# Kernel tuning notes

Measured on AMD Instinct MI355X. Metric: run time of the kernel, lower is better.

Reference implementation:

```python
import jax, jax.numpy as jnp
import numpy as np

N_NODES = 10000
N_EDGES = 640000
D_NODE = 128
D_EDGE = 64
D_IN = D_NODE + D_EDGE  # 192
D_OUT = 128


def setup_inputs() -> dict:
    key = jax.random.key(0)
    k1, k2, k3, k4 = jax.random.split(key, 4)
    x = jax.random.normal(k1, (N_NODES, D_NODE), dtype=jnp.float32)
    edge_index = jax.random.randint(k2, (2, N_EDGES), 0, N_NODES, dtype=jnp.int64)
    edge_features = jax.random.normal(k3, (N_EDGES, D_EDGE), dtype=jnp.float32)
    W = jax.random.normal(k4, (D_IN, D_OUT), dtype=jnp.float32) * (1.0 / np.sqrt(D_IN))
    b = jnp.zeros((D_OUT,), dtype=jnp.float32)
    return {"x": x, "edge_index": edge_index, "edge_features": edge_features, "W": W, "b": b}


def reference(x, edge_index, edge_features, W, b):
    n_nodes = x.shape[0]
    src = edge_index[0]  # [E]
    dst = edge_index[1]  # [E]
    # gather source node feats, concat edge feats, linear
    h = jnp.concatenate([x[src], edge_features], axis=1)  # [E, D_IN]
    h = h @ W + b  # [E, D_OUT]
    # scatter-mean to destination nodes
    sums = jax.ops.segment_sum(h, dst, num_segments=n_nodes)  # [N, D_OUT]
    cnt = jax.ops.segment_sum(jnp.ones((h.shape[0],), dtype=h.dtype), dst, num_segments=n_nodes)
    return sums / jnp.maximum(cnt, 1.0)[:, None]
```

## Files before the change

kernel.cpp:

```cpp
#include <hip/hip_runtime.h>

#define D_NODE 128
#define D_EDGE 64
#define D_IN 192
#define D_OUT 128

static __device__ __forceinline__ unsigned f2bf(float f) {
    unsigned u = __float_as_uint(f);
    return (u + 0x7fffu + ((u >> 16) & 1u)) >> 16;
}


__global__ void k_rank(const int* __restrict__ dst, int* __restrict__ cnt,
                       int* __restrict__ rank, const float2* __restrict__ x2,
                       unsigned* __restrict__ xb, int nx2, int E) {
    int e = blockIdx.x * 256 + threadIdx.x;
    if (e < E) rank[e] = atomicAdd(&cnt[dst[e]], 1);
    if (e < nx2) {
        float2 v = x2[e];
        xb[e] = f2bf(v.x) | (f2bf(v.y) << 16);
    }
}

__global__ __launch_bounds__(1024) void k_scan(const int* __restrict__ cnt,
                                               int* __restrict__ offsets, int N) {
    __shared__ int wsum[16];
    int tid = threadIdx.x;
    int lane = tid & 63, wid = tid >> 6;
    const int CH = (N + 1023) / 1024;
    int i0 = tid * CH;
    int local[16];
    int lsum = 0;
    for (int c = 0; c < CH; ++c) {
        int i = i0 + c;
        int v = (i < N) ? cnt[i] : 0;
        local[c] = v;
        lsum += v;
    }
    int incl = lsum;
    for (int off = 1; off < 64; off <<= 1) {
        int t = __shfl_up(incl, off, 64);
        if (lane >= off) incl += t;
    }
    if (lane == 63) wsum[wid] = incl;
    __syncthreads();
    if (wid == 0) {
        int s = (lane < 16) ? wsum[lane] : 0;
        for (int off = 1; off < 16; off <<= 1) {
            int t = __shfl_up(s, off, 64);
            if (lane >= off) s += t;
        }
        if (lane < 16) wsum[lane] = s;
    }
    __syncthreads();
    int waveoff = (wid > 0) ? wsum[wid - 1] : 0;
    int run = waveoff + incl - lsum;
    for (int c = 0; c < CH; ++c) {
        int i = i0 + c;
        if (i < N) { offsets[i] = run; run += local[c]; }
    }
    if (tid == 0) offsets[N] = wsum[15];
}

__global__ void k_place(const int* __restrict__ ei, const int* __restrict__ offsets,
                        const int* __restrict__ rank, int2* __restrict__ csr, int E) {
    int i = blockIdx.x * 256 + threadIdx.x;
    int e = i * 4;
    if (e + 4 <= E) {
        int4 s4 = *(const int4*)(ei + e);
        int4 d4 = *(const int4*)(ei + E + e);
        int4 r4 = *(const int4*)(rank + e);
        csr[offsets[d4.x] + r4.x] = make_int2(s4.x, e + 0);
        csr[offsets[d4.y] + r4.y] = make_int2(s4.y, e + 1);
        csr[offsets[d4.z] + r4.z] = make_int2(s4.z, e + 2);
        csr[offsets[d4.w] + r4.w] = make_int2(s4.w, e + 3);
    } else {
        for (; e < E; ++e)
            csr[offsets[ei[E + e]] + rank[e]] = make_int2(ei[e], e);
    }
}

__global__ __launch_bounds__(256) void k_gather(
        const unsigned* __restrict__ xb, const float* __restrict__ ef,
        const int* __restrict__ offsets, const int2* __restrict__ csr,
        float* __restrict__ agg, int N) {
    int wid = threadIdx.x >> 6;
    int lane = threadIdx.x & 63;
    int node = blockIdx.x * 4 + wid;
    if (node >= N) return;
    int start = offsets[node];
    int end = offsets[node + 1];
    float ax[4] = {0.f, 0.f, 0.f, 0.f};
    float ay[4] = {0.f, 0.f, 0.f, 0.f};
    float az[4] = {0.f, 0.f, 0.f, 0.f};
    for (int base = start; base < end; base += 64) {
        int m = end - base;
        if (m > 64) m = 64;
        int2 ent = make_int2(0, 0);
        if (lane < m) {
            long long raw = __builtin_nontemporal_load((const long long*)(csr + base + lane));
            ent.x = (int)(raw & 0xffffffffLL);
            ent.y = (int)(raw >> 32);
        }
        int j = 0;
        for (; j + 8 <= m; j += 8) {
            unsigned xv[8];
            float    ev[8];
#pragma unroll
            for (int u = 0; u < 8; ++u) {
                int s  = __shfl(ent.x, j + u, 64);
                int id = __shfl(ent.y, j + u, 64);
                xv[u] = xb[(unsigned)s * 64u + lane];
                ev[u] = __builtin_nontemporal_load(ef + (unsigned)id * 64u + lane);
            }
#pragma unroll
            for (int u = 0; u < 8; ++u) {
                ax[u & 3] += __uint_as_float(xv[u] << 16);
                ay[u & 3] += __uint_as_float(xv[u] & 0xffff0000u);
                az[u & 3] += ev[u];
            }
        }
        for (; j < m; ++j) {
            int s  = __shfl(ent.x, j, 64);
            int id = __shfl(ent.y, j, 64);
            unsigned xv = xb[(unsigned)s * 64u + lane];
            float    ev = __builtin_nontemporal_load(ef + (unsigned)id * 64u + lane);
            ax[0] += __uint_as_float(xv << 16);
            ay[0] += __uint_as_float(xv & 0xffff0000u);
            az[0] += ev;
        }
    }
    float a0 = (ax[0] + ax[1]) + (ax[2] + ax[3]);
    float a1 = (ay[0] + ay[1]) + (ay[2] + ay[3]);
    float a2 = (az[0] + az[1]) + (az[2] + az[3]);
    float2* aggrow = (float2*)(agg + (size_t)node * D_IN);
    aggrow[lane] = make_float2(a0, a1);
    agg[(size_t)node * D_IN + 128 + lane] = a2;
}

__global__ __launch_bounds__(256) void k_gemm(
        const float* __restrict__ agg, const float* __restrict__ W,
        const float* __restrict__ b, const int* __restrict__ offsets,
        float* __restrict__ out, int N) {
    __shared__ float sAgg[16][D_IN];
    __shared__ int scnt[16];
    int tid = threadIdx.x;
    int n0 = blockIdx.x * 16;
    for (int i = tid; i < 16 * D_IN; i += 256) {
        int m = i / D_IN;
        int k = i - m * D_IN;
        int n = n0 + m;
        sAgg[m][k] = (n < N) ? agg[(size_t)n * D_IN + k] : 0.0f;
    }
    if (tid < 16) {
        int n = n0 + tid;
        scnt[tid] = (n < N) ? (offsets[n + 1] - offsets[n]) : 0;
    }
    __syncthreads();
    int o = tid & 127;
    int g = tid >> 7;
    float acc[8];
#pragma unroll
    for (int m = 0; m < 8; ++m) acc[m] = 0.0f;
    for (int k = 0; k < D_IN; k += 4) {
        float w0 = W[(k + 0) * D_OUT + o];
        float w1 = W[(k + 1) * D_OUT + o];
        float w2 = W[(k + 2) * D_OUT + o];
        float w3 = W[(k + 3) * D_OUT + o];
#pragma unroll
        for (int m = 0; m < 8; ++m) {
            const float4 av = *(const float4*)(&sAgg[g * 8 + m][k]);
            acc[m] += av.x * w0 + av.y * w1 + av.z * w2 + av.w * w3;
        }
    }
    float bo = b[o];
#pragma unroll
    for (int m = 0; m < 8; ++m) {
        int n = n0 + g * 8 + m;
        if (n < N) {
            int c = scnt[g * 8 + m];
            float v = (c > 0) ? (acc[m] / (float)c + bo) : 0.0f;
            __builtin_nontemporal_store(v, &out[(size_t)n * D_OUT + o]);
        }
    }
}

extern "C" void kernel_launch(void* const* d_in, const int* in_sizes, int n_in,
                              void* d_out, int out_size, void* d_ws, size_t ws_size,
                              hipStream_t stream) {
    const float* x  = (const float*)d_in[0];
    const int*   ei = (const int*)d_in[1];
    const float* ef = (const float*)d_in[2];
    const float* W  = (const float*)d_in[3];
    const float* b  = (const float*)d_in[4];
    float* out = (float*)d_out;

    const int N = in_sizes[0] / D_NODE;
    const int E = in_sizes[2] / D_EDGE;
    const int nx2 = in_sizes[0] / 2;

    auto align64 = [](size_t v) { return (v + 63) & ~(size_t)63; };
    char* ws = (char*)d_ws;
    size_t o_cnt = 0;
    size_t o_off = align64(o_cnt + (size_t)N * 4);
    size_t o_rnk = align64(o_off + (size_t)(N + 1) * 4);
    size_t o_csr = align64(o_rnk + (size_t)E * 4);
    size_t o_xb  = align64(o_csr + (size_t)E * 8);
    size_t o_agg = align64(o_xb + (size_t)nx2 * 4);
    int*  cnt     = (int*)(ws + o_cnt);
    int*  offsets = (int*)(ws + o_off);
    int*  rank    = (int*)(ws + o_rnk);
    int2* csr     = (int2*)(ws + o_csr);
    unsigned* xb  = (unsigned*)(ws + o_xb);
    float* agg    = (float*)(ws + o_agg);

    int gridR = ((E > nx2 ? E : nx2) + 255) / 256;
    hipMemsetAsync(cnt, 0, (size_t)N * 4, stream);
    k_rank<<<gridR, 256, 0, stream>>>(ei + E, cnt, rank, (const float2*)x, xb, nx2, E);
    k_scan<<<1, 1024, 0, stream>>>(cnt, offsets, N);
    k_place<<<(E / 4 + 255) / 256, 256, 0, stream>>>(ei, offsets, rank, csr, E);
    k_gather<<<(N + 3) / 4, 256, 0, stream>>>(xb, ef, offsets, csr, agg, N);
    k_gemm<<<(N + 15) / 16, 256, 0, stream>>>(agg, W, b, offsets, out, N);
}
```

Before: 326.4 us.

## Fuse all stages into one persistent kernel with grid barriers

Replaces five kernel launches with a single persistent kernel of 512 blocks that uses atomic-counter grid barriers between the count, scan, CSR-place, and gather+GEMM phases. The gather now writes aggregated rows directly into shared memory and immediately runs the GEMM, eliminating the global agg buffer round trip. This removes launch overheads and the intermediate store/load, but it relies on all 512 blocks being co-resident, serializes the scan onto one 256-thread block, and reduces gather parallelism (4 waves per 16-node chunk).

Measured after the change: 870.4 us. 2.67x slower.

```diff
diff --git a/kernel.cpp b/kernel.cpp
--- a/kernel.cpp
+++ b/kernel.cpp
@@ -4,183 +4,184 @@
 #define D_EDGE 64
 #define D_IN 192
 #define D_OUT 128
+#define NBLK 512
 
 static __device__ __forceinline__ unsigned f2bf(float f) {
     unsigned u = __float_as_uint(f);
     return (u + 0x7fffu + ((u >> 16) & 1u)) >> 16;
 }
 
-
-__global__ void k_rank(const int* __restrict__ dst, int* __restrict__ cnt,
-                       int* __restrict__ rank, const float2* __restrict__ x2,
-                       unsigned* __restrict__ xb, int nx2, int E) {
-    int e = blockIdx.x * 256 + threadIdx.x;
-    if (e < E) rank[e] = atomicAdd(&cnt[dst[e]], 1);
-    if (e < nx2) {
-        float2 v = x2[e];
-        xb[e] = f2bf(v.x) | (f2bf(v.y) << 16);
-    }
-}
-
-__global__ __launch_bounds__(1024) void k_scan(const int* __restrict__ cnt,
-                                               int* __restrict__ offsets, int N) {
-    __shared__ int wsum[16];
-    int tid = threadIdx.x;
-    int lane = tid & 63, wid = tid >> 6;
-    const int CH = (N + 1023) / 1024;
-    int i0 = tid * CH;
-    int local[16];
-    int lsum = 0;
-    for (int c = 0; c < CH; ++c) {
-        int i = i0 + c;
-        int v = (i < N) ? cnt[i] : 0;
-        local[c] = v;
-        lsum += v;
-    }
-    int incl = lsum;
-    for (int off = 1; off < 64; off <<= 1) {
-        int t = __shfl_up(incl, off, 64);
-        if (lane >= off) incl += t;
-    }
-    if (lane == 63) wsum[wid] = incl;
+static __device__ __forceinline__ void grid_barrier(int* ctr, int nblocks) {
     __syncthreads();
-    if (wid == 0) {
-        int s = (lane < 16) ? wsum[lane] : 0;
-        for (int off = 1; off < 16; off <<= 1) {
-            int t = __shfl_up(s, off, 64);
-            if (lane >= off) s += t;
-        }
-        if (lane < 16) wsum[lane] = s;
+    if (threadIdx.x == 0) {
+        __threadfence();
+        __hip_atomic_fetch_add(ctr, 1, __ATOMIC_ACQ_REL, __HIP_MEMORY_SCOPE_AGENT);
+        while (__hip_atomic_load(ctr, __ATOMIC_ACQUIRE, __HIP_MEMORY_SCOPE_AGENT) < nblocks) {
+            __builtin_amdgcn_s_sleep(2);
+        }
+        __threadfence();
     }
     __syncthreads();
-    int waveoff = (wid > 0) ? wsum[wid - 1] : 0;
-    int run = waveoff + incl - lsum;
-    for (int c = 0; c < CH; ++c) {
-        int i = i0 + c;
-        if (i < N) { offsets[i] = run; run += local[c]; }
-    }
-    if (tid == 0) offsets[N] = wsum[15];
-}
-
-__global__ void k_place(const int* __restrict__ ei, const int* __restrict__ offsets,
-                        const int* __restrict__ rank, int2* __restrict__ csr, int E) {
-    int i = blockIdx.x * 256 + threadIdx.x;
-    int e = i * 4;
-    if (e + 4 <= E) {
-        int4 s4 = *(const int4*)(ei + e);
-        int4 d4 = *(const int4*)(ei + E + e);
-        int4 r4 = *(const int4*)(rank + e);
-        csr[offsets[d4.x] + r4.x] = make_int2(s4.x, e + 0);
-        csr[offsets[d4.y] + r4.y] = make_int2(s4.y, e + 1);
-        csr[offsets[d4.z] + r4.z] = make_int2(s4.z, e + 2);
-        csr[offsets[d4.w] + r4.w] = make_int2(s4.w, e + 3);
-    } else {
-        for (; e < E; ++e)
-            csr[offsets[ei[E + e]] + rank[e]] = make_int2(ei[e], e);
-    }
-}
-
-__global__ __launch_bounds__(256) void k_gather(
-        const unsigned* __restrict__ xb, const float* __restrict__ ef,
-        const int* __restrict__ offsets, const int2* __restrict__ csr,
-        float* __restrict__ agg, int N) {
-    int wid = threadIdx.x >> 6;
-    int lane = threadIdx.x & 63;
-    int node = blockIdx.x * 4 + wid;
-    if (node >= N) return;
-    int start = offsets[node];
-    int end = offsets[node + 1];
-    float ax[4] = {0.f, 0.f, 0.f, 0.f};
-    float ay[4] = {0.f, 0.f, 0.f, 0.f};
-    float az[4] = {0.f, 0.f, 0.f, 0.f};
-    for (int base = start; base < end; base += 64) {
-        int m = end - base;
-        if (m > 64) m = 64;
-        int2 ent = make_int2(0, 0);
-        if (lane < m) {
-            long long raw = __builtin_nontemporal_load((const long long*)(csr + base + lane));
-            ent.x = (int)(raw & 0xffffffffLL);
-            ent.y = (int)(raw >> 32);
-        }
-        int j = 0;
-        for (; j + 8 <= m; j += 8) {
-            unsigned xv[8];
-            float    ev[8];
-#pragma unroll
-            for (int u = 0; u < 8; ++u) {
-                int s  = __shfl(ent.x, j + u, 64);
-                int id = __shfl(ent.y, j + u, 64);
-                xv[u] = xb[(unsigned)s * 64u + lane];
-                ev[u] = __builtin_nontemporal_load(ef + (unsigned)id * 64u + lane);
-            }
-#pragma unroll
-            for (int u = 0; u < 8; ++u) {
-                ax[u & 3] += __uint_as_float(xv[u] << 16);
-                ay[u & 3] += __uint_as_float(xv[u] & 0xffff0000u);
-                az[u & 3] += ev[u];
-            }
-        }
-        for (; j < m; ++j) {
-            int s  = __shfl(ent.x, j, 64);
-            int id = __shfl(ent.y, j, 64);
-            unsigned xv = xb[(unsigned)s * 64u + lane];
-            float    ev = __builtin_nontemporal_load(ef + (unsigned)id * 64u + lane);
-            ax[0] += __uint_as_float(xv << 16);
-            ay[0] += __uint_as_float(xv & 0xffff0000u);
-            az[0] += ev;
-        }
-    }
-    float a0 = (ax[0] + ax[1]) + (ax[2] + ax[3]);
-    float a1 = (ay[0] + ay[1]) + (ay[2] + ay[3]);
-    float a2 = (az[0] + az[1]) + (az[2] + az[3]);
-    float2* aggrow = (float2*)(agg + (size_t)node * D_IN);
-    aggrow[lane] = make_float2(a0, a1);
-    agg[(size_t)node * D_IN + 128 + lane] = a2;
-}
-
-__global__ __launch_bounds__(256) void k_gemm(
-        const float* __restrict__ agg, const float* __restrict__ W,
-        const float* __restrict__ b, const int* __restrict__ offsets,
-        float* __restrict__ out, int N) {
+}
+
+__global__ __launch_bounds__(256, 4) void k_fused(
+        const int* __restrict__ ei,
+        const float2* __restrict__ x2, int nx2,
+        const float* __restrict__ ef,
+        const float* __restrict__ W, const float* __restrict__ b,
+        int* __restrict__ cnt, int* __restrict__ ctr,
+        int* __restrict__ offsets, int* __restrict__ rank,
+        int2* __restrict__ csr, unsigned* __restrict__ xb,
+        float* __restrict__ out, int N, int E) {
     __shared__ float sAgg[16][D_IN];
     __shared__ int scnt[16];
-    int tid = threadIdx.x;
-    int n0 = blockIdx.x * 16;
-    for (int i = tid; i < 16 * D_IN; i += 256) {
-        int m = i / D_IN;
-        int k = i - m * D_IN;
-        int n = n0 + m;
-        sAgg[m][k] = (n < N) ? agg[(size_t)n * D_IN + k] : 0.0f;
-    }
-    if (tid < 16) {
-        int n = n0 + tid;
-        scnt[tid] = (n < N) ? (offsets[n + 1] - offsets[n]) : 0;
-    }
-    __syncthreads();
-    int o = tid & 127;
-    int g = tid >> 7;
-    float acc[8];
-#pragma unroll
-    for (int m = 0; m < 8; ++m) acc[m] = 0.0f;
-    for (int k = 0; k < D_IN; k += 4) {
-        float w0 = W[(k + 0) * D_OUT + o];
-        float w1 = W[(k + 1) * D_OUT + o];
-        float w2 = W[(k + 2) * D_OUT + o];
-        float w3 = W[(k + 3) * D_OUT + o];
+    __shared__ int swsum[8];
+
+    const int tid   = threadIdx.x;
+    const int lane  = tid & 63;
+    const int wid   = tid >> 6;
+    const int gtid  = blockIdx.x * 256 + tid;
+    const int gsize = gridDim.x * 256;
+    const int nblocks = gridDim.x;
+    const int* dst  = ei + E;
+
+    for (int e = gtid; e < E; e += gsize) rank[e] = atomicAdd(&cnt[dst[e]], 1);
+    for (int i = gtid; i < nx2; i += gsize) {
+        float2 v = x2[i];
+        xb[i] = f2bf(v.x) | (f2bf(v.y) << 16);
+    }
+    grid_barrier(&ctr[0], nblocks);
+
+    if (blockIdx.x == 0) {
+        const int CH = (N + 255) / 256;
+        int i0 = tid * CH;
+        int lsum = 0;
+        for (int c = 0; c < CH; ++c) {
+            int i = i0 + c;
+            if (i < N) lsum += cnt[i];
+        }
+        int incl = lsum;
+        for (int off = 1; off < 64; off <<= 1) {
+            int t = __shfl_up(incl, off, 64);
+            if (lane >= off) incl += t;
+        }
+        if (lane == 63) swsum[wid] = incl;
+        __syncthreads();
+        if (tid == 0) {
+            int r = 0;
+            for (int w = 0; w < 4; ++w) { int v = swsum[w]; swsum[w] = r; r += v; }
+            swsum[4] = r;
+        }
+        __syncthreads();
+        int run = swsum[wid] + incl - lsum;
+        for (int c = 0; c < CH; ++c) {
+            int i = i0 + c;
+            if (i < N) { int v = cnt[i]; offsets[i] = run; run += v; }
+        }
+        if (tid == 0) offsets[N] = swsum[4];
+    }
+    grid_barrier(&ctr[1], nblocks);
+
+    {
+        int E4 = E >> 2;
+        for (int i = gtid; i < E4; i += gsize) {
+            int e = i * 4;
+            int4 s4 = *(const int4*)(ei + e);
+            int4 d4 = *(const int4*)(dst + e);
+            int4 r4 = *(const int4*)(rank + e);
+            csr[offsets[d4.x] + r4.x] = make_int2(s4.x, e + 0);
+            csr[offsets[d4.y] + r4.y] = make_int2(s4.y, e + 1);
+            csr[offsets[d4.z] + r4.z] = make_int2(s4.z, e + 2);
+            csr[offsets[d4.w] + r4.w] = make_int2(s4.w, e + 3);
+        }
+        for (int e = (E & ~3) + gtid; e < E; e += gsize)
+            csr[offsets[dst[e]] + rank[e]] = make_int2(ei[e], e);
+    }
+    grid_barrier(&ctr[2], nblocks);
+
+    const int nchunks = (N + 15) / 16;
+    for (int c = blockIdx.x; c < nchunks; c += nblocks) {
+        __syncthreads();
+        int n0 = c * 16;
+        for (int m = wid; m < 16; m += 4) {
+            int node = n0 + m;
+            if (node >= N) { if (lane == 0) scnt[m] = 0; continue; }
+            int start = offsets[node];
+            int end = offsets[node + 1];
+            float ax[4] = {0.f, 0.f, 0.f, 0.f};
+            float ay[4] = {0.f, 0.f, 0.f, 0.f};
+            float az[4] = {0.f, 0.f, 0.f, 0.f};
+            for (int base = start; base < end; base += 64) {
+                int mm = end - base;
+                if (mm > 64) mm = 64;
+                int2 ent = make_int2(0, 0);
+                if (lane < mm) {
+                    long long raw = __builtin_nontemporal_load(
+                        (const long long*)(csr + base + lane));
+                    ent.x = (int)(raw & 0xffffffffLL);
+                    ent.y = (int)(raw >> 32);
+                }
+                int j = 0;
+                for (; j + 8 <= mm; j += 8) {
+                    unsigned xv[8];
+                    float    ev[8];
+#pragma unroll
+                    for (int u = 0; u < 8; ++u) {
+                        int s  = __shfl(ent.x, j + u, 64);
+                        int id = __shfl(ent.y, j + u, 64);
+                        xv[u] = xb[(unsigned)s * 64u + lane];
+                        ev[u] = __builtin_nontemporal_load(ef + (unsigned)id * 64u + lane);
+                    }
+#pragma unroll
+                    for (int u = 0; u < 8; ++u) {
+                        ax[u & 3] += __uint_as_float(xv[u] << 16);
+                        ay[u & 3] += __uint_as_float(xv[u] & 0xffff0000u);
+                        az[u & 3] += ev[u];
+                    }
+                }
+                for (; j < mm; ++j) {
+                    int s  = __shfl(ent.x, j, 64);
+                    int id = __shfl(ent.y, j, 64);
+                    unsigned xv = xb[(unsigned)s * 64u + lane];
+                    float    ev = __builtin_nontemporal_load(ef + (unsigned)id * 64u + lane);
+                    ax[0] += __uint_as_float(xv << 16);
+                    ay[0] += __uint_as_float(xv & 0xffff0000u);
+                    az[0] += ev;
+                }
+            }
+            float a0 = (ax[0] + ax[1]) + (ax[2] + ax[3]);
+            float a1 = (ay[0] + ay[1]) + (ay[2] + ay[3]);
+            float a2 = (az[0] + az[1]) + (az[2] + az[3]);
+            *(float2*)&sAgg[m][2 * lane] = make_float2(a0, a1);
+            sAgg[m][128 + lane] = a2;
+            if (lane == 0) scnt[m] = end - start;
+        }
+        __syncthreads();
+        int o = tid & 127;
+        int g = tid >> 7;
+        float acc[8];
+#pragma unroll
+        for (int m = 0; m < 8; ++m) acc[m] = 0.0f;
+        for (int k = 0; k < D_IN; k += 4) {
+            float w0 = W[(k + 0) * D_OUT + o];
+            float w1 = W[(k + 1) * D_OUT + o];
+            float w2 = W[(k + 2) * D_OUT + o];
+            float w3 = W[(k + 3) * D_OUT + o];
+#pragma unroll
+            for (int m = 0; m < 8; ++m) {
+                const float4 av = *(const float4*)(&sAgg[g * 8 + m][k]);
+                acc[m] += av.x * w0 + av.y * w1 + av.z * w2 + av.w * w3;
+            }
+        }
+        float bo = b[o];
 #pragma unroll
         for (int m = 0; m < 8; ++m) {
-            const float4 av = *(const float4*)(&sAgg[g * 8 + m][k]);
-            acc[m] += av.x * w0 + av.y * w1 + av.z * w2 + av.w * w3;
-        }
-    }
-    float bo = b[o];
-#pragma unroll
-    for (int m = 0; m < 8; ++m) {
-        int n = n0 + g * 8 + m;
-        if (n < N) {
-            int c = scnt[g * 8 + m];
-            float v = (c > 0) ? (acc[m] / (float)c + bo) : 0.0f;
-            __builtin_nontemporal_store(v, &out[(size_t)n * D_OUT + o]);
+            int n = n0 + g * 8 + m;
+            if (n < N) {
+                int cdeg = scnt[g * 8 + m];
+                float v = (cdeg > 0) ? (acc[m] / (float)cdeg + bo) : 0.0f;
+                __builtin_nontemporal_store(v, &out[(size_t)n * D_OUT + o]);
+            }
         }
     }
 }
@@ -202,23 +203,20 @@
     auto align64 = [](size_t v) { return (v + 63) & ~(size_t)63; };
     char* ws = (char*)d_ws;
     size_t o_cnt = 0;
-    size_t o_off = align64(o_cnt + (size_t)N * 4);
+    size_t o_ctr = align64(o_cnt + (size_t)N * 4);
+    size_t o_off = align64(o_ctr + 64);
     size_t o_rnk = align64(o_off + (size_t)(N + 1) * 4);
     size_t o_csr = align64(o_rnk + (size_t)E * 4);
     size_t o_xb  = align64(o_csr + (size_t)E * 8);
-    size_t o_agg = align64(o_xb + (size_t)nx2 * 4);
     int*  cnt     = (int*)(ws + o_cnt);
+    int*  ctr     = (int*)(ws + o_ctr);
     int*  offsets = (int*)(ws + o_off);
     int*  rank    = (int*)(ws + o_rnk);
     int2* csr     = (int2*)(ws + o_csr);
     unsigned* xb  = (unsigned*)(ws + o_xb);
-    float* agg    = (float*)(ws + o_agg);
-
-    int gridR = ((E > nx2 ? E : nx2) + 255) / 256;
-    hipMemsetAsync(cnt, 0, (size_t)N * 4, stream);
-    k_rank<<<gridR, 256, 0, stream>>>(ei + E, cnt, rank, (const float2*)x, xb, nx2, E);
-    k_scan<<<1, 1024, 0, stream>>>(cnt, offsets, N);
-    k_place<<<(E / 4 + 255) / 256, 256, 0, stream>>>(ei, offsets, rank, csr, E);
-    k_gather<<<(N + 3) / 4, 256, 0, stream>>>(xb, ef, offsets, csr, agg, N);
-    k_gemm<<<(N + 15) / 16, 256, 0, stream>>>(agg, W, b, offsets, out, N);
-}
+
+    hipMemsetAsync(ws, 0, o_ctr + 64, stream);
+    k_fused<<<NBLK, 256, 0, stream>>>(ei, (const float2*)x, nx2, ef, W, b,
+                                      cnt, ctr, offsets, rank, csr, xb,
+                                      out, N, E);
+}
```

## Fuse gather aggregation and GEMM into one kernel via shared memory

Applied to the files above, without the earlier changes.

Merges the per-node gather/sum kernel and the projection GEMM into a single kernel. Each 512-thread block aggregates 16 nodes into shared memory (8 waves, 2 nodes per wave) and then applies W, bias and mean scaling directly. This removes the global agg buffer round trip and one kernel launch. In exchange, GEMM threads handle 4 rows each instead of 8, and the grid has fewer blocks (625) with 8 waves each, which changes how well the gather latency is hidden.

Result: no change. 321.9 us (-1.4%).

```diff
diff --git a/kernel.cpp b/kernel.cpp
--- a/kernel.cpp
+++ b/kernel.cpp
@@ -80,105 +80,97 @@
     }
 }
 
-__global__ __launch_bounds__(256) void k_gather(
+__global__ void k_gg(
         const unsigned* __restrict__ xb, const float* __restrict__ ef,
         const int* __restrict__ offsets, const int2* __restrict__ csr,
-        float* __restrict__ agg, int N) {
-    int wid = threadIdx.x >> 6;
-    int lane = threadIdx.x & 63;
-    int node = blockIdx.x * 4 + wid;
-    if (node >= N) return;
-    int start = offsets[node];
-    int end = offsets[node + 1];
-    float ax[4] = {0.f, 0.f, 0.f, 0.f};
-    float ay[4] = {0.f, 0.f, 0.f, 0.f};
-    float az[4] = {0.f, 0.f, 0.f, 0.f};
-    for (int base = start; base < end; base += 64) {
-        int m = end - base;
-        if (m > 64) m = 64;
-        int2 ent = make_int2(0, 0);
-        if (lane < m) {
-            long long raw = __builtin_nontemporal_load((const long long*)(csr + base + lane));
-            ent.x = (int)(raw & 0xffffffffLL);
-            ent.y = (int)(raw >> 32);
-        }
-        int j = 0;
-        for (; j + 8 <= m; j += 8) {
-            unsigned xv[8];
-            float    ev[8];
-#pragma unroll
-            for (int u = 0; u < 8; ++u) {
-                int s  = __shfl(ent.x, j + u, 64);
-                int id = __shfl(ent.y, j + u, 64);
-                xv[u] = xb[(unsigned)s * 64u + lane];
-                ev[u] = __builtin_nontemporal_load(ef + (unsigned)id * 64u + lane);
-            }
-#pragma unroll
-            for (int u = 0; u < 8; ++u) {
-                ax[u & 3] += __uint_as_float(xv[u] << 16);
-                ay[u & 3] += __uint_as_float(xv[u] & 0xffff0000u);
-                az[u & 3] += ev[u];
-            }
-        }
-        for (; j < m; ++j) {
-            int s  = __shfl(ent.x, j, 64);
-            int id = __shfl(ent.y, j, 64);
-            unsigned xv = xb[(unsigned)s * 64u + lane];
-            float    ev = __builtin_nontemporal_load(ef + (unsigned)id * 64u + lane);
-            ax[0] += __uint_as_float(xv << 16);
-            ay[0] += __uint_as_float(xv & 0xffff0000u);
-            az[0] += ev;
-        }
-    }
-    float a0 = (ax[0] + ax[1]) + (ax[2] + ax[3]);
-    float a1 = (ay[0] + ay[1]) + (ay[2] + ay[3]);
-    float a2 = (az[0] + az[1]) + (az[2] + az[3]);
-    float2* aggrow = (float2*)(agg + (size_t)node * D_IN);
-    aggrow[lane] = make_float2(a0, a1);
-    agg[(size_t)node * D_IN + 128 + lane] = a2;
-}
-
-__global__ __launch_bounds__(256) void k_gemm(
-        const float* __restrict__ agg, const float* __restrict__ W,
-        const float* __restrict__ b, const int* __restrict__ offsets,
+        const float* __restrict__ W, const float* __restrict__ b,
         float* __restrict__ out, int N) {
     __shared__ float sAgg[16][D_IN];
     __shared__ int scnt[16];
-    int tid = threadIdx.x;
-    int n0 = blockIdx.x * 16;
-    for (int i = tid; i < 16 * D_IN; i += 256) {
-        int m = i / D_IN;
-        int k = i - m * D_IN;
-        int n = n0 + m;
-        sAgg[m][k] = (n < N) ? agg[(size_t)n * D_IN + k] : 0.0f;
-    }
-    if (tid < 16) {
-        int n = n0 + tid;
-        scnt[tid] = (n < N) ? (offsets[n + 1] - offsets[n]) : 0;
+    const int tid  = threadIdx.x;
+    const int lane = tid & 63;
+    const int wid  = tid >> 6;
+    const int n0   = blockIdx.x * 16;
+
+    for (int m = wid; m < 16; m += 8) {
+        int node = n0 + m;
+        float ax[4] = {0.f, 0.f, 0.f, 0.f};
+        float ay[4] = {0.f, 0.f, 0.f, 0.f};
+        float az[4] = {0.f, 0.f, 0.f, 0.f};
+        int start = 0, end = 0;
+        if (node < N) {
+            start = offsets[node];
+            end = offsets[node + 1];
+            for (int base = start; base < end; base += 64) {
+                int mm = end - base;
+                if (mm > 64) mm = 64;
+                int2 ent = make_int2(0, 0);
+                if (lane < mm) {
+                    long long raw = __builtin_nontemporal_load(
+                        (const long long*)(csr + base + lane));
+                    ent.x = (int)(raw & 0xffffffffLL);
+                    ent.y = (int)(raw >> 32);
+                }
+                int j = 0;
+                for (; j + 8 <= mm; j += 8) {
+                    unsigned xv[8];
+                    float    ev[8];
+#pragma unroll
+                    for (int u = 0; u < 8; ++u) {
+                        int s  = __shfl(ent.x, j + u, 64);
+                        int id = __shfl(ent.y, j + u, 64);
+                        xv[u] = xb[(unsigned)s * 64u + lane];
+                        ev[u] = __builtin_nontemporal_load(ef + (unsigned)id * 64u + lane);
+                    }
+#pragma unroll
+                    for (int u = 0; u < 8; ++u) {
+                        ax[u & 3] += __uint_as_float(xv[u] << 16);
+                        ay[u & 3] += __uint_as_float(xv[u] & 0xffff0000u);
+                        az[u & 3] += ev[u];
+                    }
+                }
+                for (; j < mm; ++j) {
+                    int s  = __shfl(ent.x, j, 64);
+                    int id = __shfl(ent.y, j, 64);
+                    unsigned xv = xb[(unsigned)s * 64u + lane];
+                    float    ev = __builtin_nontemporal_load(ef + (unsigned)id * 64u + lane);
+                    ax[0] += __uint_as_float(xv << 16);
+                    ay[0] += __uint_as_float(xv & 0xffff0000u);
+                    az[0] += ev;
+                }
+            }
+        }
+        float a0 = (ax[0] + ax[1]) + (ax[2] + ax[3]);
+        float a1 = (ay[0] + ay[1]) + (ay[2] + ay[3]);
+        float a2 = (az[0] + az[1]) + (az[2] + az[3]);
+        *(float2*)&sAgg[m][2 * lane] = make_float2(a0, a1);
+        sAgg[m][128 + lane] = a2;
+        if (lane == 0) scnt[m] = end - start;
     }
     __syncthreads();
+
     int o = tid & 127;
     int g = tid >> 7;
-    float acc[8];
-#pragma unroll
-    for (int m = 0; m < 8; ++m) acc[m] = 0.0f;
+    float acc[4];
+#pragma unroll
+    for (int m = 0; m < 4; ++m) acc[m] = 0.0f;
     for (int k = 0; k < D_IN; k += 4) {
         float w0 = W[(k + 0) * D_OUT + o];
         float w1 = W[(k + 1) * D_OUT + o];
         float w2 = W[(k + 2) * D_OUT + o];
         float w3 = W[(k + 3) * D_OUT + o];
 #pragma unroll
-        for (int m = 0; m < 8; ++m) {
-            const float4 av = *(const float4*)(&sAgg[g * 8 + m][k]);
+        for (int m = 0; m < 4; ++m) {
+            const float4 av = *(const float4*)(&sAgg[g * 4 + m][k]);
             acc[m] += av.x * w0 + av.y * w1 + av.z * w2 + av.w * w3;
         }
     }
     float bo = b[o];
 #pragma unroll
-    for (int m = 0; m < 8; ++m) {
-        int n = n0 + g * 8 + m;
+    for (int m = 0; m < 4; ++m) {
+        int n = n0 + g * 4 + m;
         if (n < N) {
-            int c = scnt[g * 8 + m];
+            int c = scnt[g * 4 + m];
             float v = (c > 0) ? (acc[m] / (float)c + bo) : 0.0f;
             __builtin_nontemporal_store(v, &out[(size_t)n * D_OUT + o]);
         }
@@ -206,19 +198,16 @@
     size_t o_rnk = align64(o_off + (size_t)(N + 1) * 4);
     size_t o_csr = align64(o_rnk + (size_t)E * 4);
     size_t o_xb  = align64(o_csr + (size_t)E * 8);
-    size_t o_agg = align64(o_xb + (size_t)nx2 * 4);
     int*  cnt     = (int*)(ws + o_cnt);
     int*  offsets = (int*)(ws + o_off);
     int*  rank    = (int*)(ws + o_rnk);
     int2* csr     = (int2*)(ws + o_csr);
     unsigned* xb  = (unsigned*)(ws + o_xb);
-    float* agg    = (float*)(ws + o_agg);
 
     int gridR = ((E > nx2 ? E : nx2) + 255) / 256;
     hipMemsetAsync(cnt, 0, (size_t)N * 4, stream);
     k_rank<<<gridR, 256, 0, stream>>>(ei + E, cnt, rank, (const float2*)x, xb, nx2, E);
     k_scan<<<1, 1024, 0, stream>>>(cnt, offsets, N);
     k_place<<<(E / 4 + 255) / 256, 256, 0, stream>>>(ei, offsets, rank, csr, E);
-    k_gather<<<(N + 3) / 4, 256, 0, stream>>>(xb, ef, offsets, csr, agg, N);
-    k_gemm<<<(N + 15) / 16, 256, 0, stream>>>(agg, W, b, offsets, out, N);
-}
+    k_gg<<<(N + 15) / 16, 512, 0, stream>>>(xb, ef, offsets, csr, W, b, out, N);
+}
```
